# Kernel optimization log

Hardware: AMD Instinct MI355X
Metric: run time of the kernel (lower is better)

Reference implementation:

```python
import jax, jax.numpy as jnp
import numpy as np

N_NODES = 100000
N_EDGES = 1600000
IN_FEATS = 128
N_HIDDEN = 128
N_CLASSES = 40


def setup_inputs() -> dict:
    key = jax.random.key(0)
    ks = jax.random.split(key, 8)
    features = jax.random.normal(ks[0], (N_NODES, IN_FEATS), dtype=jnp.float32)
    src = jax.random.randint(ks[1], (N_EDGES,), 0, N_NODES, dtype=jnp.int32)
    dst = jax.random.randint(ks[2], (N_EDGES,), 0, N_NODES, dtype=jnp.int32)
    s = 1.0 / np.sqrt(N_HIDDEN)
    W1 = jax.random.normal(ks[3], (IN_FEATS, N_HIDDEN), dtype=jnp.float32) * s
    b1 = jnp.zeros((N_HIDDEN,), dtype=jnp.float32)
    W2 = jax.random.normal(ks[4], (N_HIDDEN, N_HIDDEN), dtype=jnp.float32) * s
    b2 = jnp.zeros((N_HIDDEN,), dtype=jnp.float32)
    W3 = jax.random.normal(ks[5], (N_HIDDEN, N_CLASSES), dtype=jnp.float32) * s
    b3 = jnp.zeros((N_CLASSES,), dtype=jnp.float32)
    return {"features": features, "src": src, "dst": dst,
            "W1": W1, "b1": b1, "W2": W2, "b2": b2, "W3": W3, "b3": b3}


def _gcn_layer(h, src, dst, W, b, activation):
    # message: copy src 'h' along edges; reduce: sum per dst node
    accum = jax.ops.segment_sum(h[src], dst, num_segments=N_NODES)  # [N, d]
    h = accum @ W + b
    if activation:
        h = jax.nn.relu(h)
    return h


def reference(features, src, dst, W1, b1, W2, b2, W3, b3):
    h = _gcn_layer(features, src, dst, W1, b1, True)
    h = _gcn_layer(h, src, dst, W2, b2, True)
    h = _gcn_layer(h, src, dst, W3, b3, False)
    return h  # [N_NODES, N_CLASSES]
```

## Files before the change

kernel.cpp:

```cpp
#include <hip/hip_runtime.h>
#include <hip/hip_bf16.h>


#define PBUCK  800
#define CAPB   4096

typedef __attribute__((ext_vector_type(8))) short short8;
typedef __attribute__((ext_vector_type(4))) float f32x4;

__device__ __forceinline__ float bflo(unsigned u) { return __uint_as_float(u << 16); }
__device__ __forceinline__ float bfhi(unsigned u) { return __uint_as_float(u & 0xffff0000u); }
__device__ __forceinline__ unsigned short f2bf(float f) {
    unsigned u = __float_as_uint(f);
    u = (u + 0x7fffu + ((u >> 16) & 1u)) >> 16;
    return (unsigned short)u;
}
__device__ __forceinline__ unsigned packbf(float a, float b) {
    return (unsigned)f2bf(a) | ((unsigned)f2bf(b) << 16);
}
__device__ __forceinline__ short8 as_short8(uint4 v) {
    union { uint4 u; short8 s; } x; x.u = v; return x.s;
}

__global__ __launch_bounds__(256) void cast_bf16(
    const float* __restrict__ in, unsigned short* __restrict__ out, int n8)
{
    int i = blockIdx.x * 256 + threadIdx.x;
    if (i >= n8) return;
    const float4* p = (const float4*)(in + (size_t)i * 8);
    float4 a = p[0], b = p[1];
    uint4 v = make_uint4(packbf(a.x, a.y), packbf(a.z, a.w),
                         packbf(b.x, b.y), packbf(b.z, b.w));
    *(uint4*)(out + (size_t)i * 8) = v;
}

__global__ __launch_bounds__(256) void pack_w(
    const float* __restrict__ W, unsigned short* __restrict__ Wp)
{
    int t = blockIdx.x * 256 + threadIdx.x;
    if (t >= 2048) return;
    int lane = t & 63, cg = (t >> 6) & 7, ks = t >> 9;
    int c = cg * 16 + (lane & 15);
    int kb = ks * 32 + (lane >> 4) * 8;
    unsigned short e[8];
    #pragma unroll
    for (int j = 0; j < 8; ++j) e[j] = f2bf(W[(size_t)(kb + j) * 128 + c]);
    uint4 v = make_uint4((unsigned)e[0] | ((unsigned)e[1] << 16),
                         (unsigned)e[2] | ((unsigned)e[3] << 16),
                         (unsigned)e[4] | ((unsigned)e[5] << 16),
                         (unsigned)e[6] | ((unsigned)e[7] << 16));
    *(uint4*)(Wp + (size_t)t * 8) = v;
}

__global__ __launch_bounds__(256) void pack_w3(
    const float* __restrict__ W, unsigned short* __restrict__ Wp)
{
    int t = blockIdx.x * 256 + threadIdx.x;
    if (t >= 768) return;
    int lane = t & 63, g = t >> 6;
    int ks = g / 3, cf = g % 3;
    int c = cf * 16 + (lane & 15);
    int kb = ks * 32 + (lane >> 4) * 8;
    unsigned short e[8];
    #pragma unroll
    for (int j = 0; j < 8; ++j)
        e[j] = (c < 40) ? f2bf(W[(size_t)(kb + j) * 40 + c]) : (unsigned short)0;
    uint4 v = make_uint4((unsigned)e[0] | ((unsigned)e[1] << 16),
                         (unsigned)e[2] | ((unsigned)e[3] << 16),
                         (unsigned)e[4] | ((unsigned)e[5] << 16),
                         (unsigned)e[6] | ((unsigned)e[7] << 16));
    *(uint4*)(Wp + (size_t)t * 8) = v;
}

__global__ __launch_bounds__(256) void init_pcur(int* __restrict__ pcur)
{
    int i = blockIdx.x * 256 + threadIdx.x;
    if (i < PBUCK) pcur[i] = i * CAPB;
}

__global__ __launch_bounds__(1024) void scatter_priv(
    const int* __restrict__ src, const int* __restrict__ dst,
    int* __restrict__ pcur, unsigned* __restrict__ rec, int n_edges)
{
    __shared__ int hist[PBUCK];
    __shared__ int base[PBUCK];
    int nb = gridDim.x;
    int chunk = (n_edges + nb - 1) / nb;
    int lo = blockIdx.x * chunk, hi = min(n_edges, lo + chunk);
    for (int i = threadIdx.x; i < PBUCK; i += 1024) hist[i] = 0;
    __syncthreads();
    for (int e = lo + threadIdx.x; e < hi; e += 1024)
        atomicAdd(&hist[dst[e] >> 7], 1);
    __syncthreads();
    for (int i = threadIdx.x; i < PBUCK; i += 1024) {
        int h = hist[i];
        base[i] = h ? atomicAdd(&pcur[i], h) : 0;
        hist[i] = 0;
    }
    __syncthreads();
    for (int e = lo + threadIdx.x; e < hi; e += 1024) {
        int d = dst[e];
        int b = d >> 7;
        int pos = base[b] + atomicAdd(&hist[b], 1);
        if (pos < (b + 1) * CAPB)
            rec[pos] = (unsigned)src[e] | ((unsigned)(d & 127) << 17);
    }
}

__global__ __launch_bounds__(1024) void bucket_scan(
    const int* __restrict__ pcur, int* __restrict__ bbase,
    int n_buckets, int* __restrict__ offs, int n_nodes)
{
    __shared__ int wsum[16];
    __shared__ int woff[16];
    int tid = threadIdx.x;
    int t = (tid < n_buckets) ? (pcur[tid] - tid * CAPB) : 0;
    int lane = tid & 63, wid = tid >> 6;
    int incl = t;
    #pragma unroll
    for (int off = 1; off < 64; off <<= 1) { int q = __shfl_up(incl, off); if (lane >= off) incl += q; }
    if (lane == 63) wsum[wid] = incl;
    __syncthreads();
    if (wid == 0) {
        int v = (lane < 16) ? wsum[lane] : 0;
        int ii = v;
        #pragma unroll
        for (int off = 1; off < 16; off <<= 1) { int q = __shfl_up(ii, off); if (lane >= off) ii += q; }
        if (lane < 16) woff[lane] = ii - v;
    }
    __syncthreads();
    int excl = woff[wid] + incl - t;
    if (tid <= n_buckets) bbase[tid] = excl;
    if (tid == n_buckets) offs[n_nodes] = excl;
}

__global__ __launch_bounds__(256) void fill_local2(
    const unsigned* __restrict__ rec, const int* __restrict__ pcur,
    const int* __restrict__ bbase, int* __restrict__ offs,
    int* __restrict__ esrc, int n_nodes)
{
    __shared__ int cnt[128];
    __shared__ int cur[128];
    __shared__ int wsum[4];
    int b = blockIdx.x;
    int node0 = b << 7;
    int nN = min(128, n_nodes - node0);
    int tid = threadIdx.x;
    if (tid < 128) cnt[tid] = 0;
    __syncthreads();
    int cbeg = b * CAPB;
    int cend = min(pcur[b], cbeg + CAPB);
    for (int i = cbeg + tid; i < cend; i += 256)
        atomicAdd(&cnt[rec[i] >> 17], 1);
    __syncthreads();
    int c = (tid < 128) ? cnt[tid] : 0;
    int lane = tid & 63, wid = tid >> 6;
    int incl = c;
    #pragma unroll
    for (int off = 1; off < 64; off <<= 1) { int q = __shfl_up(incl, off); if (lane >= off) incl += q; }
    if (lane == 63) wsum[wid] = incl;
    __syncthreads();
    int wpre = 0;
    for (int w = 0; w < wid; ++w) wpre += wsum[w];
    int excl = wpre + incl - c;
    int base = bbase[b];
    if (tid < nN) { offs[node0 + tid] = base + excl; cur[tid] = excl; }
    __syncthreads();
    for (int i = cbeg + tid; i < cend; i += 256) {
        unsigned r = rec[i];
        int pos = atomicAdd(&cur[r >> 17], 1);
        esrc[base + pos] = (int)(r & 0x1FFFFu);
    }
}

#define GATHER128_BODY(hk, e, end)                                          \
    while (e < end && (e & 3)) {                                            \
        uint4 v = *(const uint4*)(hk + (size_t)esrc[e] * 128);              \
        a0 += bflo(v.x); a1 += bfhi(v.x); a2 += bflo(v.y); a3 += bfhi(v.y); \
        a4 += bflo(v.z); a5 += bfhi(v.z); a6 += bflo(v.w); a7 += bfhi(v.w); \
        ++e;                                                                \
    }                                                                       \
    for (; e + 3 < end; e += 4) {                                           \
        int4 ss = *(const int4*)(esrc + e);                                 \
        uint4 v0 = *(const uint4*)(hk + (size_t)ss.x * 128);                \
        uint4 v1 = *(const uint4*)(hk + (size_t)ss.y * 128);                \
        uint4 v2 = *(const uint4*)(hk + (size_t)ss.z * 128);                \
        uint4 v3 = *(const uint4*)(hk + (size_t)ss.w * 128);                \
        a0 += (bflo(v0.x) + bflo(v1.x)) + (bflo(v2.x) + bflo(v3.x));        \
        a1 += (bfhi(v0.x) + bfhi(v1.x)) + (bfhi(v2.x) + bfhi(v3.x));        \
        a2 += (bflo(v0.y) + bflo(v1.y)) + (bflo(v2.y) + bflo(v3.y));        \
        a3 += (bfhi(v0.y) + bfhi(v1.y)) + (bfhi(v2.y) + bfhi(v3.y));        \
        a4 += (bflo(v0.z) + bflo(v1.z)) + (bflo(v2.z) + bflo(v3.z));        \
        a5 += (bfhi(v0.z) + bfhi(v1.z)) + (bfhi(v2.z) + bfhi(v3.z));        \
        a6 += (bflo(v0.w) + bflo(v1.w)) + (bflo(v2.w) + bflo(v3.w));        \
        a7 += (bfhi(v0.w) + bfhi(v1.w)) + (bfhi(v2.w) + bfhi(v3.w));        \
    }                                                                       \
    for (; e < end; ++e) {                                                  \
        uint4 v = *(const uint4*)(hk + (size_t)esrc[e] * 128);              \
        a0 += bflo(v.x); a1 += bfhi(v.x); a2 += bflo(v.y); a3 += bfhi(v.y); \
        a4 += bflo(v.z); a5 += bfhi(v.z); a6 += bflo(v.w); a7 += bfhi(v.w); \
    }

__global__ __launch_bounds__(256, 8) void gather_gemm_f(
    const unsigned short* __restrict__ h, const int* __restrict__ offs,
    const int* __restrict__ esrc, const unsigned short* __restrict__ Wp,
    const float* __restrict__ bias, unsigned short* __restrict__ out,
    int n_nodes)
{
    __shared__ unsigned short accb[16 * 136];
    const int tid = threadIdx.x;
    const int nl = tid >> 4;
    const int k  = tid & 15;
    const int node = blockIdx.x * 16 + nl;

    float a0 = 0.f, a1 = 0.f, a2 = 0.f, a3 = 0.f;
    float a4 = 0.f, a5 = 0.f, a6 = 0.f, a7 = 0.f;
    if (node < n_nodes) {
        const unsigned short* hk = h + k * 8;
        int e = offs[node], end = offs[node + 1];
        GATHER128_BODY(hk, e, end)
    }
    {
        uint4 v = make_uint4(packbf(a0, a1), packbf(a2, a3),
                             packbf(a4, a5), packbf(a6, a7));
        *(uint4*)(accb + nl * 136 + k * 8) = v;
    }
    __syncthreads();

    const int w = tid >> 6, l = tid & 63;
    short8 afr[4];
    #pragma unroll
    for (int ks = 0; ks < 4; ++ks)
        afr[ks] = as_short8(*(const uint4*)(
            accb + (l & 15) * 136 + ks * 32 + (l >> 4) * 8));

    const int node0 = blockIdx.x * 16;
    #pragma unroll
    for (int cf = 0; cf < 2; ++cf) {
        int cg = w * 2 + cf;
        int col = cg * 16 + (l & 15);
        float bb = bias[col];
        f32x4 vacc = { bb, bb, bb, bb };
        #pragma unroll
        for (int ks = 0; ks < 4; ++ks) {
            short8 bfr = as_short8(*(const uint4*)(Wp + (size_t)((ks * 8 + cg) * 64 + l) * 8));
            vacc = __builtin_amdgcn_mfma_f32_16x16x32_bf16(afr[ks], bfr, vacc, 0, 0, 0);
        }
        #pragma unroll
        for (int r = 0; r < 4; ++r) {
            int row = node0 + (l >> 4) * 4 + r;
            if (row < n_nodes)
                out[(size_t)row * 128 + col] = f2bf(fmaxf(vacc[r], 0.f));
        }
    }
}

__global__ __launch_bounds__(256, 8) void gather_gemm_ft(
    const unsigned short* __restrict__ h, const int* __restrict__ offs,
    const int* __restrict__ esrc, const unsigned short* __restrict__ Wp,
    const float* __restrict__ bias, const unsigned short* __restrict__ Wp3,
    unsigned short* __restrict__ tout, int n_nodes)
{
    __shared__ unsigned short accb[16 * 136];
    const int tid = threadIdx.x;
    const int nl = tid >> 4;
    const int k  = tid & 15;
    const int node = blockIdx.x * 16 + nl;

    float a0 = 0.f, a1 = 0.f, a2 = 0.f, a3 = 0.f;
    float a4 = 0.f, a5 = 0.f, a6 = 0.f, a7 = 0.f;
    if (node < n_nodes) {
        const unsigned short* hk = h + k * 8;
        int e = offs[node], end = offs[node + 1];
        GATHER128_BODY(hk, e, end)
    }
    {
        uint4 v = make_uint4(packbf(a0, a1), packbf(a2, a3),
                             packbf(a4, a5), packbf(a6, a7));
        *(uint4*)(accb + nl * 136 + k * 8) = v;
    }
    __syncthreads();

    const int w = tid >> 6, l = tid & 63;
    short8 afr[4];
    #pragma unroll
    for (int ks = 0; ks < 4; ++ks)
        afr[ks] = as_short8(*(const uint4*)(
            accb + (l & 15) * 136 + ks * 32 + (l >> 4) * 8));

    f32x4 hacc[2];
    #pragma unroll
    for (int cf = 0; cf < 2; ++cf) {
        int cg = w * 2 + cf;
        float bb = bias[cg * 16 + (l & 15)];
        f32x4 vacc = { bb, bb, bb, bb };
        #pragma unroll
        for (int ks = 0; ks < 4; ++ks) {
            short8 bfr = as_short8(*(const uint4*)(Wp + (size_t)((ks * 8 + cg) * 64 + l) * 8));
            vacc = __builtin_amdgcn_mfma_f32_16x16x32_bf16(afr[ks], bfr, vacc, 0, 0, 0);
        }
        hacc[cf] = vacc;
    }

    __syncthreads();
    #pragma unroll
    for (int cf = 0; cf < 2; ++cf) {
        int col = (w * 2 + cf) * 16 + (l & 15);
        #pragma unroll
        for (int r = 0; r < 4; ++r)
            accb[((l >> 4) * 4 + r) * 136 + col] = f2bf(fmaxf(hacc[cf][r], 0.f));
    }
    __syncthreads();

    if (w < 3) {
        short8 afr2[4];
        #pragma unroll
        for (int ks = 0; ks < 4; ++ks)
            afr2[ks] = as_short8(*(const uint4*)(
                accb + (l & 15) * 136 + ks * 32 + (l >> 4) * 8));
        f32x4 vacc = { 0.f, 0.f, 0.f, 0.f };
        #pragma unroll
        for (int ks = 0; ks < 4; ++ks) {
            short8 bfr = as_short8(*(const uint4*)(Wp3 + (size_t)((ks * 3 + w) * 64 + l) * 8));
            vacc = __builtin_amdgcn_mfma_f32_16x16x32_bf16(afr2[ks], bfr, vacc, 0, 0, 0);
        }
        int col = w * 16 + (l & 15);
        if (col < 40) {
            const int node0 = blockIdx.x * 16;
            #pragma unroll
            for (int r = 0; r < 4; ++r) {
                int row = node0 + (l >> 4) * 4 + r;
                if (row < n_nodes)
                    tout[(size_t)row * 40 + col] = f2bf(vacc[r]);
            }
        }
    }
}

__global__ __launch_bounds__(256) void gather40v(
    const unsigned short* __restrict__ t, const int* __restrict__ offs,
    const int* __restrict__ esrc, const float* __restrict__ b3,
    float* __restrict__ out, int n_nodes)
{
    int lane = threadIdx.x & 63;
    int g = lane / 10;
    int k = lane - g * 10;
    int node = blockIdx.x * 24 + (threadIdx.x >> 6) * 6 + g;
    if (g >= 6 || node >= n_nodes) return;
    float4 bv = *(const float4*)(b3 + k * 4);
    float a0 = bv.x, a1 = bv.y, a2 = bv.z, a3 = bv.w;
    int e = offs[node], end = offs[node + 1];
    while (e < end && (e & 3)) {
        uint2 v = *(const uint2*)(t + (size_t)esrc[e] * 40 + k * 4);
        a0 += bflo(v.x); a1 += bfhi(v.x); a2 += bflo(v.y); a3 += bfhi(v.y);
        ++e;
    }
    for (; e + 3 < end; e += 4) {
        int4 ss = *(const int4*)(esrc + e);
        uint2 v0 = *(const uint2*)(t + (size_t)ss.x * 40 + k * 4);
        uint2 v1 = *(const uint2*)(t + (size_t)ss.y * 40 + k * 4);
        uint2 v2 = *(const uint2*)(t + (size_t)ss.z * 40 + k * 4);
        uint2 v3 = *(const uint2*)(t + (size_t)ss.w * 40 + k * 4);
        a0 += (bflo(v0.x) + bflo(v1.x)) + (bflo(v2.x) + bflo(v3.x));
        a1 += (bfhi(v0.x) + bfhi(v1.x)) + (bfhi(v2.x) + bfhi(v3.x));
        a2 += (bflo(v0.y) + bflo(v1.y)) + (bflo(v2.y) + bflo(v3.y));
        a3 += (bfhi(v0.y) + bfhi(v1.y)) + (bfhi(v2.y) + bfhi(v3.y));
    }
    for (; e < end; ++e) {
        uint2 v = *(const uint2*)(t + (size_t)esrc[e] * 40 + k * 4);
        a0 += bflo(v.x); a1 += bfhi(v.x); a2 += bflo(v.y); a3 += bfhi(v.y);
    }
    *(float4*)(out + (size_t)node * 40 + k * 4) = make_float4(a0, a1, a2, a3);
}

extern "C" void kernel_launch(void* const* d_in, const int* in_sizes, int n_in,
                              void* d_out, int out_size, void* d_ws, size_t ws_size,
                              hipStream_t stream)
{
    const float* feat = (const float*)d_in[0];
    const int*   src  = (const int*)d_in[1];
    const int*   dst  = (const int*)d_in[2];
    const float* W1   = (const float*)d_in[3];
    const float* b1   = (const float*)d_in[4];
    const float* W2   = (const float*)d_in[5];
    const float* b2   = (const float*)d_in[6];
    const float* W3   = (const float*)d_in[7];
    const float* b3   = (const float*)d_in[8];
    float* out = (float*)d_out;

    const int n_edges = in_sizes[1];
    const int n_nodes = in_sizes[0] / 128;
    const int n_buckets = (n_nodes + 127) >> 7;

    unsigned short* SC = (unsigned short*)d_ws;
    unsigned short* SD = SC + (size_t)n_nodes * 128;
    unsigned* rec = (unsigned*)(SD + (size_t)n_nodes * 128);
    int*  esrc = (int*)(rec + (size_t)PBUCK * CAPB);
    int*  offs = esrc + n_edges;
    int*  pcur = offs + n_nodes + 1;
    int*  bbase = pcur + PBUCK;
    unsigned short* Wp1 = (unsigned short*)(bbase + n_buckets + 1);
    unsigned short* Wp2 = Wp1 + 2048 * 8;
    unsigned short* Wp3 = Wp2 + 2048 * 8;

    init_pcur<<<(PBUCK + 255) / 256, 256, 0, stream>>>(pcur);
    cast_bf16<<<(n_nodes * 16 + 255) / 256, 256, 0, stream>>>(feat, SC, n_nodes * 16);
    pack_w<<<8, 256, 0, stream>>>(W1, Wp1);
    pack_w<<<8, 256, 0, stream>>>(W2, Wp2);
    pack_w3<<<3, 256, 0, stream>>>(W3, Wp3);
    scatter_priv<<<512, 1024, 0, stream>>>(src, dst, pcur, rec, n_edges);
    bucket_scan<<<1, 1024, 0, stream>>>(pcur, bbase, n_buckets, offs, n_nodes);
    fill_local2<<<n_buckets, 256, 0, stream>>>(rec, pcur, bbase, offs, esrc, n_nodes);

    const int fg = (n_nodes + 15) / 16;

    gather_gemm_f<<<fg, 256, 0, stream>>>(SC, offs, esrc, Wp1, b1, SD, n_nodes);

    gather_gemm_ft<<<fg, 256, 0, stream>>>(SD, offs, esrc, Wp2, b2, Wp3, SC, n_nodes);

    gather40v<<<(n_nodes + 23) / 24, 256, 0, stream>>>(SC, offs, esrc, b3, out, n_nodes);
}
```

Baseline: 234.3 us.

## Sort nodes by degree for balanced gather blocks and fuse setup kernels

```diff
diff --git a/kernel.cpp b/kernel.cpp
--- a/kernel.cpp
+++ b/kernel.cpp
@@ -22,22 +22,9 @@
     union { uint4 u; short8 s; } x; x.u = v; return x.s;
 }
 
-__global__ __launch_bounds__(256) void cast_bf16(
-    const float* __restrict__ in, unsigned short* __restrict__ out, int n8)
-{
-    int i = blockIdx.x * 256 + threadIdx.x;
-    if (i >= n8) return;
-    const float4* p = (const float4*)(in + (size_t)i * 8);
-    float4 a = p[0], b = p[1];
-    uint4 v = make_uint4(packbf(a.x, a.y), packbf(a.z, a.w),
-                         packbf(b.x, b.y), packbf(b.z, b.w));
-    *(uint4*)(out + (size_t)i * 8) = v;
-}
-
-__global__ __launch_bounds__(256) void pack_w(
-    const float* __restrict__ W, unsigned short* __restrict__ Wp)
-{
-    int t = blockIdx.x * 256 + threadIdx.x;
+__device__ __forceinline__ void packw_body(
+    const float* __restrict__ W, unsigned short* __restrict__ Wp, int t)
+{
     if (t >= 2048) return;
     int lane = t & 63, cg = (t >> 6) & 7, ks = t >> 9;
     int c = cg * 16 + (lane & 15);
@@ -51,11 +38,9 @@
                          (unsigned)e[6] | ((unsigned)e[7] << 16));
     *(uint4*)(Wp + (size_t)t * 8) = v;
 }
-
-__global__ __launch_bounds__(256) void pack_w3(
-    const float* __restrict__ W, unsigned short* __restrict__ Wp)
-{
-    int t = blockIdx.x * 256 + threadIdx.x;
+__device__ __forceinline__ void packw3_body(
+    const float* __restrict__ W, unsigned short* __restrict__ Wp, int t)
+{
     if (t >= 768) return;
     int lane = t & 63, g = t >> 6;
     int ks = g / 3, cf = g % 3;
@@ -72,10 +57,37 @@
     *(uint4*)(Wp + (size_t)t * 8) = v;
 }
 
-__global__ __launch_bounds__(256) void init_pcur(int* __restrict__ pcur)
-{
-    int i = blockIdx.x * 256 + threadIdx.x;
-    if (i < PBUCK) pcur[i] = i * CAPB;
+__global__ __launch_bounds__(256) void setup_kernel(
+    const float* __restrict__ feat, unsigned short* __restrict__ SC,
+    const float* __restrict__ W1, const float* __restrict__ W2,
+    const float* __restrict__ W3,
+    unsigned short* __restrict__ Wp1, unsigned short* __restrict__ Wp2,
+    unsigned short* __restrict__ Wp3, int* __restrict__ pcur,
+    int* __restrict__ ghist, int* __restrict__ perm,
+    int n_nodes, int castBlocks, int npad)
+{
+    int b = blockIdx.x, tid = threadIdx.x;
+    if (b < castBlocks) {
+        int i = b * 256 + tid;
+        if (i < n_nodes * 16) {
+            const float4* p = (const float4*)(feat + (size_t)i * 8);
+            float4 a = p[0], bb = p[1];
+            uint4 v = make_uint4(packbf(a.x, a.y), packbf(a.z, a.w),
+                                 packbf(bb.x, bb.y), packbf(bb.z, bb.w));
+            *(uint4*)(SC + (size_t)i * 8) = v;
+        }
+        return;
+    }
+    int r = b - castBlocks;
+    if (r < 8)       packw_body(W1, Wp1, r * 256 + tid);
+    else if (r < 16) packw_body(W2, Wp2, (r - 8) * 256 + tid);
+    else if (r < 19) packw3_body(W3, Wp3, (r - 16) * 256 + tid);
+    else if (r < 23) { int i = (r - 19) * 256 + tid; if (i < PBUCK) pcur[i] = i * CAPB; }
+    else {
+        if (tid < 128) ghist[tid] = 0;
+        int idx = n_nodes + tid;
+        if (idx < npad) perm[idx] = 0x7fffffff;
+    }
 }
 
 __global__ __launch_bounds__(1024) void scatter_priv(
@@ -107,54 +119,49 @@
     }
 }
 
-__global__ __launch_bounds__(1024) void bucket_scan(
-    const int* __restrict__ pcur, int* __restrict__ bbase,
-    int n_buckets, int* __restrict__ offs, int n_nodes)
-{
-    __shared__ int wsum[16];
-    __shared__ int woff[16];
-    int tid = threadIdx.x;
-    int t = (tid < n_buckets) ? (pcur[tid] - tid * CAPB) : 0;
-    int lane = tid & 63, wid = tid >> 6;
-    int incl = t;
-    #pragma unroll
-    for (int off = 1; off < 64; off <<= 1) { int q = __shfl_up(incl, off); if (lane >= off) incl += q; }
-    if (lane == 63) wsum[wid] = incl;
-    __syncthreads();
-    if (wid == 0) {
-        int v = (lane < 16) ? wsum[lane] : 0;
-        int ii = v;
-        #pragma unroll
-        for (int off = 1; off < 16; off <<= 1) { int q = __shfl_up(ii, off); if (lane >= off) ii += q; }
-        if (lane < 16) woff[lane] = ii - v;
-    }
-    __syncthreads();
-    int excl = woff[wid] + incl - t;
-    if (tid <= n_buckets) bbase[tid] = excl;
-    if (tid == n_buckets) offs[n_nodes] = excl;
-}
-
-__global__ __launch_bounds__(256) void fill_local2(
+__global__ __launch_bounds__(512) void fill_local3(
     const unsigned* __restrict__ rec, const int* __restrict__ pcur,
-    const int* __restrict__ bbase, int* __restrict__ offs,
-    int* __restrict__ esrc, int n_nodes)
+    int* __restrict__ offs, int* __restrict__ esrc,
+    int* __restrict__ ghist, int n_buckets, int n_nodes)
 {
     __shared__ int cnt[128];
     __shared__ int cur[128];
-    __shared__ int wsum[4];
-    int b = blockIdx.x;
-    int node0 = b << 7;
-    int nN = min(128, n_nodes - node0);
-    int tid = threadIdx.x;
-    if (tid < 128) cnt[tid] = 0;
-    __syncthreads();
-    int cbeg = b * CAPB;
-    int cend = min(pcur[b], cbeg + CAPB);
-    for (int i = cbeg + tid; i < cend; i += 256)
+    __shared__ int dh[128];
+    __shared__ int wsum[8];
+    __shared__ int redA[8], redL[8];
+    const int b = blockIdx.x, tid = threadIdx.x;
+    const int lane = tid & 63, wid = tid >> 6;
+
+    int accL = 0, accA = 0;
+    for (int i = tid; i < n_buckets; i += 512) {
+        int t = min(pcur[i] - i * CAPB, CAPB);
+        accA += t;
+        if (i < b) accL += t;
+    }
+    #pragma unroll
+    for (int off = 32; off; off >>= 1) {
+        accA += __shfl_down(accA, off);
+        accL += __shfl_down(accL, off);
+    }
+    if (lane == 0) { redA[wid] = accA; redL[wid] = accL; }
+    if (tid < 128) { cnt[tid] = 0; dh[tid] = 0; }
+    __syncthreads();
+    int baseAll = 0, baseLt = 0;
+    #pragma unroll
+    for (int w = 0; w < 8; ++w) { baseAll += redA[w]; baseLt += redL[w]; }
+    if (b == 0 && tid == 0) offs[n_nodes] = baseAll;
+
+    const int node0 = b << 7;
+    const int nN = min(128, n_nodes - node0);
+    const int cbeg = b * CAPB;
+    const int cend = cbeg + min(pcur[b] - cbeg, CAPB);
+
+    for (int i = cbeg + tid; i < cend; i += 512)
         atomicAdd(&cnt[rec[i] >> 17], 1);
     __syncthreads();
+
+    if (tid < nN) atomicAdd(&dh[min(cnt[tid], 127)], 1);
     int c = (tid < 128) ? cnt[tid] : 0;
-    int lane = tid & 63, wid = tid >> 6;
     int incl = c;
     #pragma unroll
     for (int off = 1; off < 64; off <<= 1) { int q = __shfl_up(incl, off); if (lane >= off) incl += q; }
@@ -163,13 +170,60 @@
     int wpre = 0;
     for (int w = 0; w < wid; ++w) wpre += wsum[w];
     int excl = wpre + incl - c;
-    int base = bbase[b];
-    if (tid < nN) { offs[node0 + tid] = base + excl; cur[tid] = excl; }
-    __syncthreads();
-    for (int i = cbeg + tid; i < cend; i += 256) {
+    if (tid < nN) { offs[node0 + tid] = baseLt + excl; cur[tid] = excl; }
+    if (tid < 128 && dh[tid]) atomicAdd(&ghist[tid], dh[tid]);
+    __syncthreads();
+
+    for (int i = cbeg + tid; i < cend; i += 512) {
         unsigned r = rec[i];
         int pos = atomicAdd(&cur[r >> 17], 1);
-        esrc[base + pos] = (int)(r & 0x1FFFFu);
+        esrc[baseLt + pos] = (int)(r & 0x1FFFFu);
+    }
+}
+
+__global__ __launch_bounds__(128) void deg_scan(
+    const int* __restrict__ ghist, int* __restrict__ gcur)
+{
+    __shared__ int ws[2];
+    int tid = threadIdx.x;
+    int t = ghist[tid];
+    int lane = tid & 63, wid = tid >> 6;
+    int incl = t;
+    #pragma unroll
+    for (int off = 1; off < 64; off <<= 1) { int q = __shfl_up(incl, off); if (lane >= off) incl += q; }
+    if (lane == 63) ws[wid] = incl;
+    __syncthreads();
+    int excl = (wid ? ws[0] : 0) + incl - t;
+    gcur[tid] = excl;
+}
+
+__global__ __launch_bounds__(256) void deg_place(
+    const int* __restrict__ offs, int* __restrict__ gcur,
+    int* __restrict__ perm, int n_nodes)
+{
+    __shared__ int dh[128];
+    __shared__ int dbase[128];
+    int nb = gridDim.x;
+    int chunk = (n_nodes + nb - 1) / nb;
+    int lo = blockIdx.x * chunk, hi = min(n_nodes, lo + chunk);
+    int tid = threadIdx.x;
+    if (tid < 128) dh[tid] = 0;
+    __syncthreads();
+    for (int n = lo + tid; n < hi; n += 256) {
+        int d = min(offs[n + 1] - offs[n], 127);
+        atomicAdd(&dh[d], 1);
+    }
+    __syncthreads();
+    if (tid < 128) {
+        int h = dh[tid];
+        dbase[tid] = h ? atomicAdd(&gcur[tid], h) : 0;
+        dh[tid] = 0;
+    }
+    __syncthreads();
+    for (int n = lo + tid; n < hi; n += 256) {
+        int d = min(offs[n + 1] - offs[n], 127);
+        int pos = dbase[d] + atomicAdd(&dh[d], 1);
+        perm[pos] = n;
     }
 }
 
@@ -203,15 +257,16 @@
 
 __global__ __launch_bounds__(256, 8) void gather_gemm_f(
     const unsigned short* __restrict__ h, const int* __restrict__ offs,
-    const int* __restrict__ esrc, const unsigned short* __restrict__ Wp,
-    const float* __restrict__ bias, unsigned short* __restrict__ out,
-    int n_nodes)
+    const int* __restrict__ esrc, const int* __restrict__ perm,
+    const unsigned short* __restrict__ Wp, const float* __restrict__ bias,
+    unsigned short* __restrict__ out, int n_nodes)
 {
     __shared__ unsigned short accb[16 * 136];
     const int tid = threadIdx.x;
     const int nl = tid >> 4;
     const int k  = tid & 15;
-    const int node = blockIdx.x * 16 + nl;
+    const int node0 = blockIdx.x * 16;
+    const int node = perm[node0 + nl];
 
     float a0 = 0.f, a1 = 0.f, a2 = 0.f, a3 = 0.f;
     float a4 = 0.f, a5 = 0.f, a6 = 0.f, a7 = 0.f;
@@ -234,7 +289,6 @@
         afr[ks] = as_short8(*(const uint4*)(
             accb + (l & 15) * 136 + ks * 32 + (l >> 4) * 8));
 
-    const int node0 = blockIdx.x * 16;
     #pragma unroll
     for (int cf = 0; cf < 2; ++cf) {
         int cg = w * 2 + cf;
@@ -248,24 +302,26 @@
         }
         #pragma unroll
         for (int r = 0; r < 4; ++r) {
-            int row = node0 + (l >> 4) * 4 + r;
-            if (row < n_nodes)
-                out[(size_t)row * 128 + col] = f2bf(fmaxf(vacc[r], 0.f));
+            int prow = perm[node0 + (l >> 4) * 4 + r];
+            if (prow < n_nodes)
+                out[(size_t)prow * 128 + col] = f2bf(fmaxf(vacc[r], 0.f));
         }
     }
 }
 
 __global__ __launch_bounds__(256, 8) void gather_gemm_ft(
     const unsigned short* __restrict__ h, const int* __restrict__ offs,
-    const int* __restrict__ esrc, const unsigned short* __restrict__ Wp,
-    const float* __restrict__ bias, const unsigned short* __restrict__ Wp3,
+    const int* __restrict__ esrc, const int* __restrict__ perm,
+    const unsigned short* __restrict__ Wp, const float* __restrict__ bias,
+    const unsigned short* __restrict__ Wp3,
     unsigned short* __restrict__ tout, int n_nodes)
 {
     __shared__ unsigned short accb[16 * 136];
     const int tid = threadIdx.x;
     const int nl = tid >> 4;
     const int k  = tid & 15;
-    const int node = blockIdx.x * 16 + nl;
+    const int node0 = blockIdx.x * 16;
+    const int node = perm[node0 + nl];
 
     float a0 = 0.f, a1 = 0.f, a2 = 0.f, a3 = 0.f;
     float a4 = 0.f, a5 = 0.f, a6 = 0.f, a7 = 0.f;
@@ -326,12 +382,11 @@
         }
         int col = w * 16 + (l & 15);
         if (col < 40) {
-            const int node0 = blockIdx.x * 16;
             #pragma unroll
             for (int r = 0; r < 4; ++r) {
-                int row = node0 + (l >> 4) * 4 + r;
-                if (row < n_nodes)
-                    tout[(size_t)row * 40 + col] = f2bf(vacc[r]);
+                int prow = perm[node0 + (l >> 4) * 4 + r];
+                if (prow < n_nodes)
+                    tout[(size_t)prow * 40 + col] = f2bf(vacc[r]);
             }
         }
     }
@@ -339,14 +394,17 @@
 
 __global__ __launch_bounds__(256) void gather40v(
     const unsigned short* __restrict__ t, const int* __restrict__ offs,
-    const int* __restrict__ esrc, const float* __restrict__ b3,
-    float* __restrict__ out, int n_nodes)
+    const int* __restrict__ esrc, const int* __restrict__ perm,
+    const float* __restrict__ b3, float* __restrict__ out,
+    int n_nodes, int npad)
 {
     int lane = threadIdx.x & 63;
     int g = lane / 10;
     int k = lane - g * 10;
-    int node = blockIdx.x * 24 + (threadIdx.x >> 6) * 6 + g;
-    if (g >= 6 || node >= n_nodes) return;
+    int slot = blockIdx.x * 24 + (threadIdx.x >> 6) * 6 + g;
+    if (g >= 6 || slot >= npad) return;
+    int node = perm[slot];
+    if (node >= n_nodes) return;
     float4 bv = *(const float4*)(b3 + k * 4);
     float a0 = bv.x, a1 = bv.y, a2 = bv.z, a3 = bv.w;
     int e = offs[node], end = offs[node + 1];
@@ -391,6 +449,8 @@
     const int n_edges = in_sizes[1];
     const int n_nodes = in_sizes[0] / 128;
     const int n_buckets = (n_nodes + 127) >> 7;
+    const int fg = (n_nodes + 15) / 16;
+    const int npad = fg * 16;
 
     unsigned short* SC = (unsigned short*)d_ws;
     unsigned short* SD = SC + (size_t)n_nodes * 128;
@@ -398,25 +458,28 @@
     int*  esrc = (int*)(rec + (size_t)PBUCK * CAPB);
     int*  offs = esrc + n_edges;
     int*  pcur = offs + n_nodes + 1;
-    int*  bbase = pcur + PBUCK;
-    unsigned short* Wp1 = (unsigned short*)(bbase + n_buckets + 1);
+    unsigned short* Wp1 = (unsigned short*)(pcur + PBUCK);
     unsigned short* Wp2 = Wp1 + 2048 * 8;
     unsigned short* Wp3 = Wp2 + 2048 * 8;
-
-    init_pcur<<<(PBUCK + 255) / 256, 256, 0, stream>>>(pcur);
-    cast_bf16<<<(n_nodes * 16 + 255) / 256, 256, 0, stream>>>(feat, SC, n_nodes * 16);
-    pack_w<<<8, 256, 0, stream>>>(W1, Wp1);
-    pack_w<<<8, 256, 0, stream>>>(W2, Wp2);
-    pack_w3<<<3, 256, 0, stream>>>(W3, Wp3);
+    int* ghist = (int*)(Wp3 + 768 * 8);
+    int* gcur  = ghist + 128;
+    int* perm  = gcur + 128;
+
+    const int castBlocks = (n_nodes * 16 + 255) / 256;
+
+    setup_kernel<<<castBlocks + 24, 256, 0, stream>>>(
+        feat, SC, W1, W2, W3, Wp1, Wp2, Wp3, pcur, ghist, perm,
+        n_nodes, castBlocks, npad);
     scatter_priv<<<512, 1024, 0, stream>>>(src, dst, pcur, rec, n_edges);
-    bucket_scan<<<1, 1024, 0, stream>>>(pcur, bbase, n_buckets, offs, n_nodes);
-    fill_local2<<<n_buckets, 256, 0, stream>>>(rec, pcur, bbase, offs, esrc, n_nodes);
-
-    const int fg = (n_nodes + 15) / 16;
-
-    gather_gemm_f<<<fg, 256, 0, stream>>>(SC, offs, esrc, Wp1, b1, SD, n_nodes);
-
-    gather_gemm_ft<<<fg, 256, 0, stream>>>(SD, offs, esrc, Wp2, b2, Wp3, SC, n_nodes);
-
-    gather40v<<<(n_nodes + 23) / 24, 256, 0, stream>>>(SC, offs, esrc, b3, out, n_nodes);
-}
+    fill_local3<<<n_buckets, 512, 0, stream>>>(rec, pcur, offs, esrc, ghist,
+                                               n_buckets, n_nodes);
+    deg_scan<<<1, 128, 0, stream>>>(ghist, gcur);
+    deg_place<<<256, 256, 0, stream>>>(offs, gcur, perm, n_nodes);
+
+    gather_gemm_f<<<fg, 256, 0, stream>>>(SC, offs, esrc, perm, Wp1, b1, SD, n_nodes);
+
+    gather_gemm_ft<<<fg, 256, 0, stream>>>(SD, offs, esrc, perm, Wp2, b2, Wp3, SC, n_nodes);
+
+    gather40v<<<(npad + 23) / 24, 256, 0, stream>>>(SC, offs, esrc, perm, b3, out,
+                                                    n_nodes, npad);
+}
```

Measured after the change: 246.5 us. 1.05x slower.
